# Optimization experiments

Measured on AMD Instinct MI355X. Metric: run time of the kernel, lower is better.

Reference implementation:

```python
import jax, jax.numpy as jnp
import numpy as np

B, S, D = 2, 2048, 768
H = 12
DK = D // H  # 64; dim_q = dim_k = dim_v
DFF = 3072
EPS = 1e-5


def layer_norm(x, w, b):
    mu = jnp.mean(x, axis=-1, keepdims=True)
    var = jnp.var(x, axis=-1, keepdims=True)
    return (x - mu) * jax.lax.rsqrt(var + EPS) * w + b


def setup_inputs() -> dict:
    key = jax.random.key(0)
    ks = jax.random.split(key, 12)
    s = 0.02
    return {
        "src": jax.random.normal(ks[0], (B, S, D), dtype=jnp.float32),
        # per-head projections stacked over heads: [H, D, DK]
        "Wq": jax.random.normal(ks[1], (H, D, DK), dtype=jnp.float32) * s,
        "bq": jnp.zeros((H, DK), dtype=jnp.float32),
        "Wk": jax.random.normal(ks[2], (H, D, DK), dtype=jnp.float32) * s,
        "bk": jnp.zeros((H, DK), dtype=jnp.float32),
        "Wv": jax.random.normal(ks[3], (H, D, DK), dtype=jnp.float32) * s,
        "bv": jnp.zeros((H, DK), dtype=jnp.float32),
        # output projection: [H*DK, D]
        "Wo": jax.random.normal(ks[4], (H * DK, D), dtype=jnp.float32) * s,
        "bo": jnp.zeros((D,), dtype=jnp.float32),
        "ln1_w": jnp.ones((D,), dtype=jnp.float32),
        "ln1_b": jnp.zeros((D,), dtype=jnp.float32),
        "W1": jax.random.normal(ks[5], (D, DFF), dtype=jnp.float32) * s,
        "b1": jnp.zeros((DFF,), dtype=jnp.float32),
        "W2": jax.random.normal(ks[6], (DFF, D), dtype=jnp.float32) * s,
        "b2": jnp.zeros((D,), dtype=jnp.float32),
        "ln2_w": jnp.ones((D,), dtype=jnp.float32),
        "ln2_b": jnp.zeros((D,), dtype=jnp.float32),
    }


def reference(src, Wq, bq, Wk, bk, Wv, bv, Wo, bo, ln1_w, ln1_b,
              W1, b1, W2, b2, ln2_w, ln2_b):
    # per-head q/k/v projections, batched over heads via einsum
    q = jnp.einsum('bsd,hdk->bhsk', src, Wq) + bq[None, :, None, :]
    k = jnp.einsum('bsd,hdk->bhsk', src, Wk) + bk[None, :, None, :]
    v = jnp.einsum('bsd,hdk->bhsk', src, Wv) + bv[None, :, None, :]
    scale = jnp.asarray(DK, src.dtype) ** 0.5
    scores = jnp.einsum('bhsk,bhtk->bhst', q, k) / scale  # [B,H,S,S]
    attn = jax.nn.softmax(scores, axis=-1)
    ctx = jnp.einsum('bhst,bhtk->bhsk', attn, v)
    # concat heads along feature dim (matches torch.cat over head outputs)
    ctx = ctx.transpose(0, 2, 1, 3).reshape(src.shape[0], src.shape[1], H * DK)
    attn_out = ctx @ Wo + bo
    x = layer_norm(src + attn_out, ln1_w, ln1_b)
    ff = jax.nn.relu(x @ W1 + b1) @ W2 + b2
    return layer_norm(x + ff, ln2_w, ln2_b)
```

## Files before the change

kernel.cpp:

```cpp
#include <hip/hip_runtime.h>
#include <hip/hip_bf16.h>

#define S_LEN 2048
#define DMODEL 768
#define NHEAD 12
#define DKH 64
#define DFF_K 3072
#define MROWS 4096

typedef __attribute__((ext_vector_type(8))) short bf16x8;
typedef __attribute__((ext_vector_type(8))) unsigned short us8;
typedef __attribute__((ext_vector_type(4))) float f32x4;

__device__ __forceinline__ float bfu2f(unsigned short u) {
  return __uint_as_float(((unsigned int)u) << 16);
}
__device__ __forceinline__ unsigned short f2bfu(float f) {
  __hip_bfloat16 h = __float2bfloat16(f);
  return *reinterpret_cast<unsigned short*>(&h);
}

__global__ __launch_bounds__(256) void convert_kernel(
    const float* __restrict__ in, unsigned short* __restrict__ out, int n4)
{
  const int i = blockIdx.x * 256 + threadIdx.x;
  if (i < n4) {
    float4 v = *(const float4*)(in + (size_t)i * 4);
    ushort4 o;
    o.x = f2bfu(v.x); o.y = f2bfu(v.y); o.z = f2bfu(v.z); o.w = f2bfu(v.w);
    *(ushort4*)(out + (size_t)i * 4) = o;
  }
}

__device__ __forceinline__ void transpose_conv_body(
    const float* in, unsigned short* out, int R, int Ctot, int head,
    int bx, int by, int tid)
{
  __shared__ float t[64][68];
  const int r0 = bx * 64;
  const int c0 = by * 64;
  const float* ib;
  int ld;
  if (head) { ib = in + (size_t)by * R * 64; ld = 64; }
  else      { ib = in + c0;                  ld = Ctot; }
  const int lr = tid >> 4;
  const int lc = (tid & 15) << 2;

#pragma unroll
  for (int rr = 0; rr < 4; ++rr) {
    const int row = rr * 16 + lr;
    float4 v = *(const float4*)(ib + (size_t)(r0 + row) * ld + lc);
    t[row][lc + 0] = v.x; t[row][lc + 1] = v.y;
    t[row][lc + 2] = v.z; t[row][lc + 3] = v.w;
  }
  __syncthreads();
#pragma unroll
  for (int rr = 0; rr < 4; ++rr) {
    const int oc = rr * 16 + lr;
    ushort4 o;
    o.x = f2bfu(t[lc + 0][oc]); o.y = f2bfu(t[lc + 1][oc]);
    o.z = f2bfu(t[lc + 2][oc]); o.w = f2bfu(t[lc + 3][oc]);
    *(ushort4*)(out + (size_t)(c0 + oc) * R + r0 + lc) = o;
  }
}

__global__ __launch_bounds__(256) void transpose_conv_kernel(
    const float* __restrict__ in, unsigned short* __restrict__ out,
    int R, int Ctot, int head)
{
  transpose_conv_body(in, out, R, Ctot, head, blockIdx.x, blockIdx.y, threadIdx.x);
}

__global__ __launch_bounds__(256) void transpose_conv4_kernel(
    const float* __restrict__ i0, const float* __restrict__ i1,
    const float* __restrict__ i2, const float* __restrict__ i3,
    unsigned short* __restrict__ o0, unsigned short* __restrict__ o1,
    unsigned short* __restrict__ o2, unsigned short* __restrict__ o3)
{
  const int z = blockIdx.z;
  const float* in = (z == 0) ? i0 : (z == 1) ? i1 : (z == 2) ? i2 : i3;
  unsigned short* out = (z == 0) ? o0 : (z == 1) ? o1 : (z == 2) ? o2 : o3;
  transpose_conv_body(in, out, DMODEL, DMODEL, (z < 3) ? 1 : 0,
                      blockIdx.x, blockIdx.y, threadIdx.x);
}

template<int BN>
__global__ __launch_bounds__(256) void mfma_gemm_kernel(
    const unsigned short* __restrict__ A,
    const unsigned short* __restrict__ BT,
    const float* __restrict__ bias,
    unsigned short* __restrict__ C,
    int K, int N, int relu, int klen, size_t out_stride)
{
  constexpr int WN = (BN == 128) ? 64 : 32;
  constexpr int NJ = WN / 16;
  __shared__ unsigned short As[128][40];
  __shared__ unsigned short Bs[BN][40];

  const int tid  = threadIdx.x;
  const int wid  = tid >> 6;
  const int lane = tid & 63;
  const int ml   = lane & 15;
  const int quad = lane >> 4;
  const int wm   = (wid & 1) * 64;
  const int wn   = (wid >> 1) * WN;
  const int row0 = blockIdx.x * 128;
  const int col0 = blockIdx.y * BN;
  const int zed  = blockIdx.z;
  const int kb0  = zed * klen;
  const int kend = kb0 + klen;

  const int sr = tid >> 2;
  const int sk = (tid & 3) << 3;

  const unsigned short* pA0 = A  + (size_t)(row0 + sr) * K + sk;
  const unsigned short* pA1 = A  + (size_t)(row0 + sr + 64) * K + sk;
  const unsigned short* pB0 = BT + (size_t)(col0 + sr) * K + sk;
  const unsigned short* pB1 = BT + (size_t)(col0 + sr + 64) * K + sk;

  f32x4 acc[4][NJ];
#pragma unroll
  for (int i = 0; i < 4; ++i)
#pragma unroll
    for (int j = 0; j < NJ; ++j)
#pragma unroll
      for (int r = 0; r < 4; ++r) acc[i][j][r] = 0.f;

  us8 ra0 = *(const us8*)(pA0 + kb0);
  us8 ra1 = *(const us8*)(pA1 + kb0);
  us8 rb0 = *(const us8*)(pB0 + kb0);
  us8 rb1;
  if (BN == 128) rb1 = *(const us8*)(pB1 + kb0);

  for (int k0 = kb0; k0 < kend; k0 += 32) {
    *(us8*)&As[sr][sk]      = ra0;
    *(us8*)&As[sr + 64][sk] = ra1;
    *(us8*)&Bs[sr][sk]      = rb0;
    if (BN == 128) *(us8*)&Bs[sr + 64][sk] = rb1;
    __syncthreads();

    const int kn = k0 + 32;
    if (kn < kend) {
      ra0 = *(const us8*)(pA0 + kn);
      ra1 = *(const us8*)(pA1 + kn);
      rb0 = *(const us8*)(pB0 + kn);
      if (BN == 128) rb1 = *(const us8*)(pB1 + kn);
    }

    bf16x8 af[4], bfr[NJ];
#pragma unroll
    for (int i = 0; i < 4; ++i)
      af[i] = *(const bf16x8*)&As[wm + i * 16 + ml][quad << 3];
#pragma unroll
    for (int j = 0; j < NJ; ++j)
      bfr[j] = *(const bf16x8*)&Bs[wn + j * 16 + ml][quad << 3];
#pragma unroll
    for (int i = 0; i < 4; ++i)
#pragma unroll
      for (int j = 0; j < NJ; ++j)
        acc[i][j] = __builtin_amdgcn_mfma_f32_16x16x32_bf16(
            af[i], bfr[j], acc[i][j], 0, 0, 0);
    __syncthreads();
  }

  unsigned short* Cz = C + (size_t)zed * out_stride;
#pragma unroll
  for (int j = 0; j < NJ; ++j) {
    const int col = col0 + wn + j * 16 + ml;
    const float bb = (zed == 0) ? bias[col] : 0.f;
#pragma unroll
    for (int i = 0; i < 4; ++i) {
      const int r0g = row0 + wm + i * 16 + (quad << 2);
#pragma unroll
      for (int r = 0; r < 4; ++r) {
        float v = acc[i][j][r] + bb;
        if (relu) v = fmaxf(v, 0.f);
        Cz[(size_t)(r0g + r) * N + col] = f2bfu(v);
      }
    }
  }
}

__global__ __launch_bounds__(256) void qkv_gemm_kernel(
    const unsigned short* __restrict__ A,
    const unsigned short* __restrict__ W0, const unsigned short* __restrict__ W1,
    const unsigned short* __restrict__ W2,
    const float* __restrict__ bq, const float* __restrict__ bk,
    const float* __restrict__ bv,
    unsigned short* __restrict__ C0, unsigned short* __restrict__ C1,
    unsigned short* __restrict__ C2)
{
  __shared__ unsigned short As[128][40];
  __shared__ unsigned short Bs[64][40];
  const int z = blockIdx.z;
  const unsigned short* BT = (z == 0) ? W0 : (z == 1) ? W1 : W2;
  const float* bias = (z == 0) ? bq : (z == 1) ? bk : bv;
  unsigned short* C = (z == 0) ? C0 : (z == 1) ? C1 : C2;
  const int K = DMODEL, N = DMODEL;

  const int tid  = threadIdx.x;
  const int wid  = tid >> 6;
  const int lane = tid & 63;
  const int ml   = lane & 15;
  const int quad = lane >> 4;
  const int wm   = (wid & 1) * 64;
  const int wn   = (wid >> 1) * 32;
  const int row0 = blockIdx.x * 128;
  const int col0 = blockIdx.y * 64;
  const int sr = tid >> 2;
  const int sk = (tid & 3) << 3;

  const unsigned short* pA0 = A  + (size_t)(row0 + sr) * K + sk;
  const unsigned short* pA1 = A  + (size_t)(row0 + sr + 64) * K + sk;
  const unsigned short* pB0 = BT + (size_t)(col0 + sr) * K + sk;

  f32x4 acc[4][2];
#pragma unroll
  for (int i = 0; i < 4; ++i)
#pragma unroll
    for (int j = 0; j < 2; ++j)
#pragma unroll
      for (int r = 0; r < 4; ++r) acc[i][j][r] = 0.f;

  us8 ra0 = *(const us8*)pA0;
  us8 ra1 = *(const us8*)pA1;
  us8 rb0 = *(const us8*)pB0;

  for (int k0 = 0; k0 < K; k0 += 32) {
    *(us8*)&As[sr][sk]      = ra0;
    *(us8*)&As[sr + 64][sk] = ra1;
    *(us8*)&Bs[sr][sk]      = rb0;
    __syncthreads();

    const int kn = k0 + 32;
    if (kn < K) {
      ra0 = *(const us8*)(pA0 + kn);
      ra1 = *(const us8*)(pA1 + kn);
      rb0 = *(const us8*)(pB0 + kn);
    }

    bf16x8 af[4], bfr[2];
#pragma unroll
    for (int i = 0; i < 4; ++i)
      af[i] = *(const bf16x8*)&As[wm + i * 16 + ml][quad << 3];
#pragma unroll
    for (int j = 0; j < 2; ++j)
      bfr[j] = *(const bf16x8*)&Bs[wn + j * 16 + ml][quad << 3];
#pragma unroll
    for (int i = 0; i < 4; ++i)
#pragma unroll
      for (int j = 0; j < 2; ++j)
        acc[i][j] = __builtin_amdgcn_mfma_f32_16x16x32_bf16(
            af[i], bfr[j], acc[i][j], 0, 0, 0);
    __syncthreads();
  }

#pragma unroll
  for (int j = 0; j < 2; ++j) {
    const int col = col0 + wn + j * 16 + ml;
    const float bb = bias[col];
#pragma unroll
    for (int i = 0; i < 4; ++i) {
      const int r0g = row0 + wm + i * 16 + (quad << 2);
      if (z == 2) {
        const int bb_ = r0g >> 11, s = r0g & 2047;
        const int hh = col >> 6, dd = col & 63;
        ushort4 o;
        o.x = f2bfu(acc[i][j][0] + bb); o.y = f2bfu(acc[i][j][1] + bb);
        o.z = f2bfu(acc[i][j][2] + bb); o.w = f2bfu(acc[i][j][3] + bb);
        *(ushort4*)(C + ((size_t)((bb_ * NHEAD + hh) * DKH + dd)) * S_LEN + s) = o;
      } else {
#pragma unroll
        for (int r = 0; r < 4; ++r)
          C[(size_t)(r0g + r) * N + col] = f2bfu(acc[i][j][r] + bb);
      }
    }
  }
}

#define FATS 72
#define SCL2E 0.1803368822f
__global__ __launch_bounds__(256) void flash_attn_mfma(
    const unsigned short* __restrict__ Q,
    const unsigned short* __restrict__ K,
    const unsigned short* __restrict__ VT,
    unsigned short* __restrict__ O)
{
  __shared__ unsigned short Ks[64][FATS];
  __shared__ unsigned short Vs[64][FATS];
  __shared__ unsigned short QP[4][16][FATS];

  const int tid  = threadIdx.x;
  const int wid  = tid >> 6;
  const int lane = tid & 63;
  const int ml   = lane & 15;
  const int quad = lane >> 4;
  const int h    = blockIdx.x, b = blockIdx.y;
  const int q0   = blockIdx.z * 64;

  const size_t qkbase = ((size_t)b * S_LEN) * DMODEL + (size_t)h * DKH;
  const size_t vtbase = ((size_t)(b * NHEAD + h)) * DKH * S_LEN;

  const int sr = tid >> 2;
  const int sc = (tid & 3) << 4;

  {
    const unsigned short* qp = Q + qkbase + (size_t)(q0 + sr) * DMODEL + sc;
    *(us8*)&QP[sr >> 4][sr & 15][sc]     = *(const us8*)qp;
    *(us8*)&QP[sr >> 4][sr & 15][sc + 8] = *(const us8*)(qp + 8);
  }
  bf16x8 qf[2];
  qf[0] = *(const bf16x8*)&QP[wid][ml][quad << 3];
  qf[1] = *(const bf16x8*)&QP[wid][ml][32 + (quad << 3)];

  const unsigned short* pK = K + qkbase + (size_t)sr * DMODEL + sc;
  const unsigned short* pV = VT + vtbase + (size_t)sr * S_LEN + sc;

  float lsum = 0.f;
  f32x4 oacc[4];
#pragma unroll
  for (int dt = 0; dt < 4; ++dt)
#pragma unroll
    for (int r = 0; r < 4; ++r) oacc[dt][r] = 0.f;

  us8 rk0 = *(const us8*)(pK);
  us8 rk1 = *(const us8*)(pK + 8);
  us8 rv0 = *(const us8*)(pV);
  us8 rv1 = *(const us8*)(pV + 8);

  for (int kt = 0; kt < S_LEN; kt += 64) {
    __syncthreads();
    *(us8*)&Ks[sr][sc]     = rk0;
    *(us8*)&Ks[sr][sc + 8] = rk1;
    *(us8*)&Vs[sr][sc]     = rv0;
    *(us8*)&Vs[sr][sc + 8] = rv1;
    __syncthreads();

    const int ktn = kt + 64;
    if (ktn < S_LEN) {
      rk0 = *(const us8*)(pK + (size_t)ktn * DMODEL);
      rk1 = *(const us8*)(pK + (size_t)ktn * DMODEL + 8);
      rv0 = *(const us8*)(pV + ktn);
      rv1 = *(const us8*)(pV + ktn + 8);
    }

    f32x4 sacc[4];
#pragma unroll
    for (int mt = 0; mt < 4; ++mt)
#pragma unroll
      for (int r = 0; r < 4; ++r) sacc[mt][r] = 0.f;
#pragma unroll
    for (int mt = 0; mt < 4; ++mt) {
      bf16x8 kf0 = *(const bf16x8*)&Ks[mt * 16 + ml][quad << 3];
      bf16x8 kf1 = *(const bf16x8*)&Ks[mt * 16 + ml][32 + (quad << 3)];
      sacc[mt] = __builtin_amdgcn_mfma_f32_16x16x32_bf16(kf0, qf[0], sacc[mt], 0, 0, 0);
      sacc[mt] = __builtin_amdgcn_mfma_f32_16x16x32_bf16(kf1, qf[1], sacc[mt], 0, 0, 0);
    }

    float p[4][4];
#pragma unroll
    for (int mt2 = 0; mt2 < 4; ++mt2)
#pragma unroll
      for (int r = 0; r < 4; ++r) {
        const float e = exp2f(sacc[mt2][r] * SCL2E);
        p[mt2][r] = e;
        lsum += e;
      }

#pragma unroll
    for (int mt2 = 0; mt2 < 4; ++mt2) {
      ushort4 o;
      o.x = f2bfu(p[mt2][0]); o.y = f2bfu(p[mt2][1]);
      o.z = f2bfu(p[mt2][2]); o.w = f2bfu(p[mt2][3]);
      *(ushort4*)&QP[wid][ml][mt2 * 16 + (quad << 2)] = o;
    }
    bf16x8 pf0 = *(const bf16x8*)&QP[wid][ml][quad << 3];
    bf16x8 pf1 = *(const bf16x8*)&QP[wid][ml][32 + (quad << 3)];

#pragma unroll
    for (int dt = 0; dt < 4; ++dt) {
      bf16x8 vf0 = *(const bf16x8*)&Vs[dt * 16 + ml][quad << 3];
      bf16x8 vf1 = *(const bf16x8*)&Vs[dt * 16 + ml][32 + (quad << 3)];
      oacc[dt] = __builtin_amdgcn_mfma_f32_16x16x32_bf16(vf0, pf0, oacc[dt], 0, 0, 0);
      oacc[dt] = __builtin_amdgcn_mfma_f32_16x16x32_bf16(vf1, pf1, oacc[dt], 0, 0, 0);
    }
  }

  lsum += __shfl_xor(lsum, 16);
  lsum += __shfl_xor(lsum, 32);
  const float inv = 1.f / lsum;
  const int qrow = q0 + wid * 16 + ml;
#pragma unroll
  for (int dt = 0; dt < 4; ++dt)
#pragma unroll
    for (int r = 0; r < 4; ++r)
      O[qkbase + (size_t)qrow * DMODEL + dt * 16 + (quad << 2) + r] =
          f2bfu(oacc[dt][r] * inv);
}

__global__ __launch_bounds__(256) void add_ln_kernel(
    const void* __restrict__ X, const void* __restrict__ Y,
    const void* __restrict__ Y2,
    const float* __restrict__ w, const float* __restrict__ bvec,
    void* __restrict__ out, int xbf, int ybf, int obf)
{
  __shared__ float buf[DMODEL];
  __shared__ float rbuf[8];
  const int tid  = threadIdx.x;
  const int lane = tid & 63, wv = tid >> 6;
  const size_t base = (size_t)blockIdx.x * DMODEL;

  float s = 0.f, s2 = 0.f;
#pragma unroll
  for (int j = tid; j < DMODEL; j += 256) {
    float xv = xbf ? bfu2f(((const unsigned short*)X)[base + j])
                   : ((const float*)X)[base + j];
    float yv = ybf ? bfu2f(((const unsigned short*)Y)[base + j])
                   : ((const float*)Y)[base + j];
    float v = xv + yv;
    if (Y2) v += ybf ? bfu2f(((const unsigned short*)Y2)[base + j])
                     : ((const float*)Y2)[base + j];
    buf[j] = v; s += v; s2 += v * v;
  }
#pragma unroll
  for (int o = 32; o; o >>= 1) { s += __shfl_xor(s, o); s2 += __shfl_xor(s2, o); }
  if (lane == 0) { rbuf[wv] = s; rbuf[4 + wv] = s2; }
  __syncthreads();
  const float S  = rbuf[0] + rbuf[1] + rbuf[2] + rbuf[3];
  const float S2 = rbuf[4] + rbuf[5] + rbuf[6] + rbuf[7];
  const float mean = S * (1.f / (float)DMODEL);
  const float var  = S2 * (1.f / (float)DMODEL) - mean * mean;
  const float rstd = rsqrtf(var + 1e-5f);
#pragma unroll
  for (int j = tid; j < DMODEL; j += 256) {
    float v = (buf[j] - mean) * rstd * w[j] + bvec[j];
    if (obf) ((unsigned short*)out)[base + j] = f2bfu(v);
    else     ((float*)out)[base + j] = v;
  }
}

extern "C" void kernel_launch(void* const* d_in, const int* in_sizes, int n_in,
                              void* d_out, int out_size, void* d_ws, size_t ws_size,
                              hipStream_t stream) {
  const float* src  = (const float*)d_in[0];
  const float* Wq   = (const float*)d_in[1];
  const float* bq   = (const float*)d_in[2];
  const float* Wk   = (const float*)d_in[3];
  const float* bk   = (const float*)d_in[4];
  const float* Wv   = (const float*)d_in[5];
  const float* bv   = (const float*)d_in[6];
  const float* Wo   = (const float*)d_in[7];
  const float* bo   = (const float*)d_in[8];
  const float* ln1w = (const float*)d_in[9];
  const float* ln1b = (const float*)d_in[10];
  const float* W1   = (const float*)d_in[11];
  const float* b1   = (const float*)d_in[12];
  const float* W2   = (const float*)d_in[13];
  const float* b2   = (const float*)d_in[14];
  const float* ln2w = (const float*)d_in[15];
  const float* ln2b = (const float*)d_in[16];
  (void)ws_size; (void)in_sizes; (void)n_in; (void)out_size;

  unsigned short* p = (unsigned short*)d_ws;
  const size_t SEG = (size_t)MROWS * DMODEL;
  unsigned short* srcb = p; p += SEG;
  unsigned short* qb   = p; p += SEG;
  unsigned short* kb_  = p; p += SEG;
  unsigned short* vbT  = p; p += SEG;
  unsigned short* ctx  = p; p += SEG;
  unsigned short* ff   = p; p += (size_t)MROWS * DFF_K;
  unsigned short* wqt  = p; p += (size_t)DMODEL * DMODEL;
  unsigned short* wkt  = p; p += (size_t)DMODEL * DMODEL;
  unsigned short* wvt  = p; p += (size_t)DMODEL * DMODEL;
  unsigned short* wot  = p; p += (size_t)DMODEL * DMODEL;
  unsigned short* w1t  = p; p += (size_t)DMODEL * DFF_K;
  unsigned short* w2t  = p; p += (size_t)DMODEL * DFF_K;
  unsigned short* x1 = kb_;

  dim3 blk(256);

  convert_kernel<<<dim3(SEG / 1024), blk, 0, stream>>>(src, srcb, (int)(SEG / 4));
  transpose_conv4_kernel<<<dim3(12, 12, 4), blk, 0, stream>>>(
      Wq, Wk, Wv, Wo, wqt, wkt, wvt, wot);
  transpose_conv_kernel<<<dim3(12, 48), blk, 0, stream>>>(W1, w1t, DMODEL, DFF_K, 0);
  transpose_conv_kernel<<<dim3(48, 12), blk, 0, stream>>>(W2, w2t, DFF_K, DMODEL, 0);

  dim3 gqkv(MROWS / 128, DMODEL / 64, 3);
  qkv_gemm_kernel<<<gqkv, blk, 0, stream>>>(srcb, wqt, wkt, wvt, bq, bk, bv,
                                            qb, kb_, vbT);

  dim3 ga(NHEAD, 2, S_LEN / 64);
  flash_attn_mfma<<<ga, blk, 0, stream>>>(qb, kb_, vbT, ctx);

  dim3 gWo(MROWS / 128, DMODEL / 64, 2);
  mfma_gemm_kernel<64><<<gWo, blk, 0, stream>>>(ctx, wot, bo, qb,
                                                DMODEL, DMODEL, 0, DMODEL / 2, 2 * SEG);

  add_ln_kernel<<<dim3(MROWS), blk, 0, stream>>>(srcb, qb, vbT,
                                                 ln1w, ln1b, x1, 1, 1, 1);

  dim3 gF1(MROWS / 128, DFF_K / 128, 1);
  mfma_gemm_kernel<128><<<gF1, blk, 0, stream>>>(x1, w1t, b1, ff,
                                                 DMODEL, DFF_K, 1, DMODEL, 0);

  dim3 gW2(MROWS / 128, DMODEL / 64, 2);
  mfma_gemm_kernel<64><<<gW2, blk, 0, stream>>>(ff, w2t, b2, qb,
                                                DFF_K, DMODEL, 0, DFF_K / 2, 2 * SEG);

  add_ln_kernel<<<dim3(MROWS), blk, 0, stream>>>(x1, qb, vbT,
                                                 ln2w, ln2b, (float*)d_out, 1, 1, 0);
}
```

Before: 306.9 us.

## Split attention key range in two and combine partial results

The flash attention kernel now runs twice as many blocks. Each block covers half the key sequence and writes unnormalised fp32 partial outputs and row sums into scratch space that reuses the FF and weight buffers. A new combine kernel adds the two partials and divides by the summed normaliser to produce the bf16 context. This is meant to raise parallelism and shorten the serial key loop per block. In exchange it adds roughly 25MB of fp32 partial traffic and an extra kernel launch.

```diff
diff --git a/kernel.cpp b/kernel.cpp
--- a/kernel.cpp
+++ b/kernel.cpp
@@ -7,6 +7,8 @@
 #define DKH 64
 #define DFF_K 3072
 #define MROWS 4096
+#define KSPLIT 2
+#define KHALF (S_LEN / KSPLIT)
 
 typedef __attribute__((ext_vector_type(8))) short bf16x8;
 typedef __attribute__((ext_vector_type(8))) unsigned short us8;
@@ -284,7 +286,8 @@
     const unsigned short* __restrict__ Q,
     const unsigned short* __restrict__ K,
     const unsigned short* __restrict__ VT,
-    unsigned short* __restrict__ O)
+    float* __restrict__ Opart,
+    float* __restrict__ Lpart)
 {
   __shared__ unsigned short Ks[64][FATS];
   __shared__ unsigned short Vs[64][FATS];
@@ -296,7 +299,9 @@
   const int ml   = lane & 15;
   const int quad = lane >> 4;
   const int h    = blockIdx.x, b = blockIdx.y;
-  const int q0   = blockIdx.z * 64;
+  const int q0   = (blockIdx.z >> 1) * 64;
+  const int ks   = blockIdx.z & 1;
+  const int kt0  = ks * KHALF;
 
   const size_t qkbase = ((size_t)b * S_LEN) * DMODEL + (size_t)h * DKH;
   const size_t vtbase = ((size_t)(b * NHEAD + h)) * DKH * S_LEN;
@@ -313,8 +318,8 @@
   qf[0] = *(const bf16x8*)&QP[wid][ml][quad << 3];
   qf[1] = *(const bf16x8*)&QP[wid][ml][32 + (quad << 3)];
 
-  const unsigned short* pK = K + qkbase + (size_t)sr * DMODEL + sc;
-  const unsigned short* pV = VT + vtbase + (size_t)sr * S_LEN + sc;
+  const unsigned short* pK = K + qkbase + (size_t)(kt0 + sr) * DMODEL + sc;
+  const unsigned short* pV = VT + vtbase + (size_t)sr * S_LEN + kt0 + sc;
 
   float lsum = 0.f;
   f32x4 oacc[4];
@@ -328,7 +333,7 @@
   us8 rv0 = *(const us8*)(pV);
   us8 rv1 = *(const us8*)(pV + 8);
 
-  for (int kt = 0; kt < S_LEN; kt += 64) {
+  for (int kt = 0; kt < KHALF; kt += 64) {
     __syncthreads();
     *(us8*)&Ks[sr][sc]     = rk0;
     *(us8*)&Ks[sr][sc + 8] = rk1;
@@ -337,7 +342,7 @@
     __syncthreads();
 
     const int ktn = kt + 64;
-    if (ktn < S_LEN) {
+    if (ktn < KHALF) {
       rk0 = *(const us8*)(pK + (size_t)ktn * DMODEL);
       rk1 = *(const us8*)(pK + (size_t)ktn * DMODEL + 8);
       rv0 = *(const us8*)(pV + ktn);
@@ -388,14 +393,35 @@
 
   lsum += __shfl_xor(lsum, 16);
   lsum += __shfl_xor(lsum, 32);
-  const float inv = 1.f / lsum;
   const int qrow = q0 + wid * 16 + ml;
+  const size_t obase =
+      ((((size_t)(ks * 2 + b)) * NHEAD + h) * S_LEN + qrow) * DKH;
 #pragma unroll
   for (int dt = 0; dt < 4; ++dt)
-#pragma unroll
-    for (int r = 0; r < 4; ++r)
-      O[qkbase + (size_t)qrow * DMODEL + dt * 16 + (quad << 2) + r] =
-          f2bfu(oacc[dt][r] * inv);
+    *(f32x4*)&Opart[obase + dt * 16 + (quad << 2)] = oacc[dt];
+  if (quad == 0)
+    Lpart[(((size_t)(ks * 2 + b)) * NHEAD + h) * S_LEN + qrow] = lsum;
+}
+
+__global__ __launch_bounds__(256) void attn_combine_kernel(
+    const float* __restrict__ Op,
+    const float* __restrict__ Lp,
+    unsigned short* __restrict__ O)
+{
+  const int s = blockIdx.x & (S_LEN - 1);
+  const int b = blockIdx.x >> 11;
+  const int tid = threadIdx.x;
+  const size_t ohalf = (size_t)2 * NHEAD * S_LEN * DKH;
+  const size_t lhalf = (size_t)2 * NHEAD * S_LEN;
+#pragma unroll
+  for (int c = tid; c < DMODEL; c += 256) {
+    const int hh = c >> 6, dd = c & 63;
+    const size_t li = ((size_t)b * NHEAD + hh) * S_LEN + s;
+    const size_t oi = li * DKH + dd;
+    const float o = Op[oi] + Op[ohalf + oi];
+    const float l = Lp[li] + Lp[lhalf + li];
+    O[((size_t)b * S_LEN + s) * DMODEL + c] = f2bfu(o / l);
+  }
 }
 
 __global__ __launch_bounds__(256) void add_ln_kernel(
@@ -476,6 +502,8 @@
   unsigned short* w1t  = p; p += (size_t)DMODEL * DFF_K;
   unsigned short* w2t  = p; p += (size_t)DMODEL * DFF_K;
   unsigned short* x1 = kb_;
+  float* opart = (float*)ff;
+  float* lpart = (float*)wqt;
 
   dim3 blk(256);
 
@@ -489,8 +517,9 @@
   qkv_gemm_kernel<<<gqkv, blk, 0, stream>>>(srcb, wqt, wkt, wvt, bq, bk, bv,
                                             qb, kb_, vbT);
 
-  dim3 ga(NHEAD, 2, S_LEN / 64);
-  flash_attn_mfma<<<ga, blk, 0, stream>>>(qb, kb_, vbT, ctx);
+  dim3 ga(NHEAD, 2, (S_LEN / 64) * KSPLIT);
+  flash_attn_mfma<<<ga, blk, 0, stream>>>(qb, kb_, vbT, opart, lpart);
+  attn_combine_kernel<<<dim3(MROWS), blk, 0, stream>>>(opart, lpart, ctx);
 
   dim3 gWo(MROWS / 128, DMODEL / 64, 2);
   mfma_gemm_kernel<64><<<gWo, blk, 0, stream>>>(ctx, wot, bo, qb,
```

New measurement: 305.9 us. Within noise of the previous version (-0.3%).
